# Kernel optimization log

Measured on AMD Instinct MI355X. Metric: run time of the kernel, lower is better.

The kernel has to match this reference:

```python
import jax, jax.numpy as jnp
import numpy as np

K_BINS = 2048
EMB_WIDTH = 512


def setup_inputs() -> dict:
    key = jax.random.key(0)
    k1, k2 = jax.random.split(key)
    x = jax.random.normal(k1, (16, EMB_WIDTH, 8192), dtype=jnp.float32)
    k = jax.random.normal(k2, (K_BINS, EMB_WIDTH), dtype=jnp.float32)
    return {"x": x, "k": k}


def reference(x, k):
    # BottleneckBlock.forward (eval path: codebook k given, no EMA update)
    N, W, T = x.shape  # W == emb_width
    # preprocess: [N, W, T] -> [N*T, W]
    xf = jnp.transpose(x, (0, 2, 1)).reshape(-1, W)
    n_el = float(xf.shape[0] * xf.shape[1])
    prenorm = jnp.linalg.norm(xf - jnp.mean(xf)) / np.float32(np.sqrt(n_el))
    # quantise: squared-distance via expansion, then argmin over codes
    x2 = jnp.sum(xf * xf, axis=-1, keepdims=True)          # [NT, 1]
    k2 = jnp.sum(k * k, axis=-1)                           # [K]
    dist = x2 - 2.0 * (xf @ k.T) + k2[None, :]             # [NT, K]
    x_l = jnp.argmin(dist, axis=-1)                        # [NT]
    fit = jnp.mean(jnp.min(dist, axis=-1))
    # dequantise: embedding gather
    x_d = k[x_l]                                           # [NT, W]
    # commit loss: ||sg(x_d) - x||^2 / numel (torch.norm(.)**2 == sum of squares)
    commit_loss = jnp.sum((jax.lax.stop_gradient(x_d) - xf) ** 2) / n_el
    # straight-through estimator
    x_q = xf + jax.lax.stop_gradient(x_d - xf)
    # postprocess: back to [N, T] and [N, W, T]
    x_l = x_l.reshape(N, T)
    x_q = jnp.transpose(x_q.reshape(N, T, W), (0, 2, 1))
    return (x_l, x_q, commit_loss, fit, prenorm)
```

## Files before the change

### kernel.cpp

```cpp
#include <hip/hip_runtime.h>

#define NBATCH 16
#define WEMB   512
#define TLEN   8192
#define KBINS  2048
#define NTROWS (NBATCH * TLEN)
#define XQN    (NBATCH * WEMB * TLEN)
#define XQ_OFF ((size_t)NTROWS)
#define SC_OFF ((size_t)NTROWS + (size_t)XQN)

#define FIX_CAP  65536
#define FIX2_CAP 8192
#define MARGIN1  0.2f
#define MARGIN2  0.02f

#define R      64
#define XS_ROW 512

typedef _Float16 half8 __attribute__((ext_vector_type(8)));
typedef __attribute__((ext_vector_type(8))) short short8;
typedef __attribute__((ext_vector_type(4))) float f32x4;

__device__ float          g_k2[KBINS];
__device__ double         g_fitp[2048];
__device__ double         g_pnp[2 * 2048];
__device__ int            g_idx[NTROWS];
__device__ int            g_list[FIX_CAP];
__device__ int            g_nfix;
__device__ int            g_list2[FIX2_CAP];
__device__ int            g_nfix2;
__device__ unsigned short g_kh[KBINS * WEMB];
__device__ unsigned short g_kbh[KBINS * WEMB];
__device__ unsigned short g_kbl[KBINS * WEMB];

static __device__ __forceinline__ unsigned short f2h(float f) {
  _Float16 h = (_Float16)f;
  unsigned short u;
  __builtin_memcpy(&u, &h, 2);
  return u;
}
static __device__ __forceinline__ unsigned short f2bf(float f) {
  unsigned int u;
  __builtin_memcpy(&u, &f, 4);
  return (unsigned short)((u + 0x7FFFu + ((u >> 16) & 1u)) >> 16);
}
static __device__ __forceinline__ float bf2f(unsigned short h) {
  unsigned int u = ((unsigned int)h) << 16;
  float f;
  __builtin_memcpy(&f, &u, 4);
  return f;
}

__global__ void zero_kernel() { g_nfix = 0; g_nfix2 = 0; }

__global__ __launch_bounds__(256) void k2_kernel(const float* __restrict__ k) {
  const int c = blockIdx.x * 4 + (threadIdx.x >> 6);
  const int lane = threadIdx.x & 63;
  const float4* kr = (const float4*)(k + (size_t)c * WEMB);
  float s = 0.f;
#pragma unroll
  for (int i = 0; i < 2; ++i) {
    float4 v = kr[lane + 64 * i];
    s += v.x * v.x + v.y * v.y + v.z * v.z + v.w * v.w;
  }
#pragma unroll
  for (int m = 1; m < 64; m <<= 1) s += __shfl_xor(s, m);
  if (lane == 0) g_k2[c] = s;
}

__global__ __launch_bounds__(256) void kprep_kernel(const float* __restrict__ k) {
  const int i = blockIdx.x * 256 + threadIdx.x;
  float4 v = ((const float4*)k)[i];
  ushort4 hf, hb, lb;
  hf.x = f2h(v.x); hb.x = f2bf(v.x); lb.x = f2bf(v.x - bf2f(hb.x));
  hf.y = f2h(v.y); hb.y = f2bf(v.y); lb.y = f2bf(v.y - bf2f(hb.y));
  hf.z = f2h(v.z); hb.z = f2bf(v.z); lb.z = f2bf(v.z - bf2f(hb.z));
  hf.w = f2h(v.w); hb.w = f2bf(v.w); lb.w = f2bf(v.w - bf2f(hb.w));
  ((ushort4*)g_kh)[i]  = hf;
  ((ushort4*)g_kbh)[i] = hb;
  ((ushort4*)g_kbl)[i] = lb;
}

__global__ __launch_bounds__(1024, 8) void vq_mfma(const float* __restrict__ x) {
  __shared__ unsigned short x_s[R * XS_ROW];
  __shared__ float  cand_d1[16][R];
  __shared__ float  cand_d2[16][R];
  __shared__ int    cand_i[16][R];
  __shared__ float  x2s[R];
  __shared__ double pnred[32];

  const int tid = threadIdx.x;
  const int wv = tid >> 6, lane = tid & 63;
  const int g = lane >> 4, i16 = lane & 15;
  const int rows0 = blockIdx.x * R;
  const int n = rows0 >> 13, t0 = rows0 & (TLEN - 1);
  const int swz = (i16 & 7) << 3;

  {
    float sv = 0.f, px = 0.f;
    const size_t xb = ((size_t)(n * WEMB + wv * 32)) * TLEN + (size_t)(t0 + lane);
    const int wsz = (lane & 7) << 3;
#pragma unroll
    for (int jg = 0; jg < 4; ++jg) {
      half8 h8;
#pragma unroll
      for (int j = 0; j < 8; ++j) {
        const float v = __builtin_nontemporal_load(&x[xb + (size_t)(jg * 8 + j) * TLEN]);
        h8[j] = (_Float16)v;
        px = fmaf(v, v, px);
        sv += v;
      }
      const int col = wv * 32 + jg * 8;
      *(half8*)&x_s[lane * XS_ROW + (col ^ wsz)] = h8;
    }
    cand_d1[wv][lane] = px;
    float svr = sv, pxr = px;
#pragma unroll
    for (int m = 1; m < 64; m <<= 1) { svr += __shfl_xor(svr, m); pxr += __shfl_xor(pxr, m); }
    if (lane == 0) { pnred[wv] = (double)svr; pnred[16 + wv] = (double)pxr; }
  }
  __syncthreads();
  if (tid < R) {
    float t = 0.f;
#pragma unroll
    for (int w16 = 0; w16 < 16; ++w16) t += cand_d1[w16][tid];
    x2s[tid] = t;
  }
  if (tid == 0) {
    double a = 0, b = 0;
#pragma unroll
    for (int w16 = 0; w16 < 16; ++w16) { a += pnred[w16]; b += pnred[16 + w16]; }
    g_pnp[2 * blockIdx.x] = a; g_pnp[2 * blockIdx.x + 1] = b;
  }
  __syncthreads();

  cand_d1[wv][lane] = 3.4e38f;
  cand_d2[wv][lane] = 3.4e38f;
  cand_i [wv][lane] = 0x7FFFFFFF;

  for (int cc = 0; cc < 8; ++cc) {
    const int cb = cc * 256 + wv * 16;
    f32x4 acc[4];
#pragma unroll
    for (int mt = 0; mt < 4; ++mt) acc[mt] = (f32x4){0.f, 0.f, 0.f, 0.f};

#pragma unroll 1
    for (int ks = 0; ks < 16; ++ks) {
      const half8 ak = *(const half8*)&g_kh[((size_t)(cb + i16)) * WEMB + (size_t)(ks * 32 + g * 8)];
#pragma unroll
      for (int mt = 0; mt < 4; ++mt) {
        const half8 bx = *(const half8*)&x_s[(mt * 16 + i16) * XS_ROW + ((ks * 32 + g * 8) ^ swz)];
        acc[mt] = __builtin_amdgcn_mfma_f32_16x16x32_f16(ak, bx, acc[mt], 0, 0, 0);
      }
    }

    float k2r[4];
#pragma unroll
    for (int r = 0; r < 4; ++r) k2r[r] = g_k2[cb + g * 4 + r];
#pragma unroll
    for (int mt = 0; mt < 4; ++mt) {
      const int row = mt * 16 + i16;
      const float xx = x2s[row];
      float e1 = 3.4e38f, e2 = 3.4e38f; int ei = 0x7FFFFFFF;
#pragma unroll
      for (int r = 0; r < 4; ++r) {
        const float d = fmaf(-2.f, acc[mt][r], xx) + k2r[r];
        const int code = cb + g * 4 + r;
        if (d < e1) { e2 = e1; e1 = d; ei = code; } else e2 = fminf(e2, d);
      }
#pragma unroll
      for (int m = 16; m <= 32; m <<= 1) {
        const float o1 = __shfl_xor(e1, m);
        const float o2 = __shfl_xor(e2, m);
        const int   oi = __shfl_xor(ei, m);
        if (o1 < e1)      { e2 = fminf(e1, o2); e1 = o1; ei = oi; }
        else if (o1 > e1) { e2 = fminf(e2, o1); }
        else              { e2 = fminf(e2, o2); if (oi < ei) ei = oi; }
      }
      if (g == 0) {
        const float c1 = cand_d1[wv][row], c2 = cand_d2[wv][row];
        const int ci = cand_i[wv][row];
        if (e1 < c1)      { cand_d2[wv][row] = fminf(c1, e2); cand_d1[wv][row] = e1; cand_i[wv][row] = ei; }
        else if (e1 > c1) { cand_d2[wv][row] = fminf(c2, e1); }
        else              { cand_d2[wv][row] = fminf(c2, e2); if (ei < ci) cand_i[wv][row] = ei; }
      }
    }
  }

  __syncthreads();
  if (tid < R) {
    float m1 = 3.4e38f, m2 = 3.4e38f; int mi = 0x7FFFFFFF;
#pragma unroll
    for (int w16 = 0; w16 < 16; ++w16) {
      const float c1 = cand_d1[w16][tid], c2 = cand_d2[w16][tid];
      const int ci = cand_i[w16][tid];
      if (c1 < m1)      { m2 = fminf(m1, c2); m1 = c1; mi = ci; }
      else if (c1 > m1) { m2 = fminf(m2, c1); }
      else              { m2 = fminf(m2, c2); if (ci < mi) mi = ci; }
    }
    const int grow = rows0 + tid;
    g_idx[grow] = mi;
    if (m2 - m1 < MARGIN1) {
      const int pos = atomicAdd(&g_nfix, 1);
      if (pos < FIX_CAP) g_list[pos] = grow;
    }
    double fs = (double)m1;
#pragma unroll
    for (int m = 1; m < 64; m <<= 1) fs += __shfl_xor(fs, m);
    if (tid == 0) g_fitp[blockIdx.x] = fs;
  }
}

__global__ __launch_bounds__(1024, 1) void fix1_mfma(const float* __restrict__ x) {
  __shared__ short  x_s[64 * 1024];
  __shared__ float  cand_d1[16][64];
  __shared__ float  cand_d2[16][64];
  __shared__ int    cand_i[16][64];
  __shared__ float  x2s[64];
  __shared__ float  rd1[64], rd2[64];
  __shared__ int    ri1[64];

  const int tid = threadIdx.x;
  const int wv = tid >> 6, lane = tid & 63;
  const int g = lane >> 4, i16 = lane & 15;
  const int swz = (i16 & 7) << 3;
  const int nfix = g_nfix < FIX_CAP ? g_nfix : FIX_CAP;

  for (int base = blockIdx.x * 64; base < nfix; base += gridDim.x * 64) {
    __syncthreads();
    if (tid < 64) { rd1[tid] = 3.4e38f; rd2[tid] = 3.4e38f; ri1[tid] = 0; }
    {
      const int rl = tid >> 4;
      int e = base + rl; if (e >= nfix) e = nfix - 1;
      const int row = g_list[e];
      const int n = row >> 13, t = row & (TLEN - 1);
      const int ks = tid & 15;
      const int wsz = (rl & 7) << 3;
      float px = 0.f;
#pragma unroll
      for (int jg = 0; jg < 4; ++jg) {
        short8 h8, l8;
#pragma unroll
        for (int j = 0; j < 8; ++j) {
          const int w = ks * 32 + jg * 8 + j;
          const float v = x[((size_t)(n * WEMB + w)) * TLEN + (size_t)t];
          const unsigned short h = f2bf(v);
          const unsigned short lo = f2bf(v - bf2f(h));
          h8[j] = (short)h; l8[j] = (short)lo;
          px = fmaf(v, v, px);
        }
        const int colh = ks * 64 + jg * 8;
        *(short8*)&x_s[rl * 1024 + (colh ^ wsz)] = h8;
        *(short8*)&x_s[rl * 1024 + ((colh + 32) ^ wsz)] = l8;
      }
#pragma unroll
      for (int m = 1; m < 16; m <<= 1) px += __shfl_xor(px, m);
      if (ks == 0) x2s[rl] = px;
    }
    __syncthreads();

    for (int cc = 0; cc < 4; ++cc) {
      const int cb = cc * 512 + wv * 32;
      f32x4 acc[4][2];
#pragma unroll
      for (int mt = 0; mt < 4; ++mt)
#pragma unroll
        for (int nt = 0; nt < 2; ++nt) acc[mt][nt] = (f32x4){0.f, 0.f, 0.f, 0.f};

#pragma unroll 1
      for (int ks = 0; ks < 16; ++ks) {
        short8 bh[2], bl[2];
#pragma unroll
        for (int nt = 0; nt < 2; ++nt) {
          const size_t bidx = ((size_t)(cb + nt * 16 + i16)) * WEMB + (size_t)(ks * 32 + g * 8);
          bh[nt] = *(const short8*)&g_kbh[bidx];
          bl[nt] = *(const short8*)&g_kbl[bidx];
        }
#pragma unroll
        for (int mt = 0; mt < 4; ++mt) {
          const int rbase = (mt * 16 + i16) * 1024 + (ks * 64);
          const short8 ah = *(const short8*)&x_s[rbase + ((g * 8) ^ swz)];
          const short8 al = *(const short8*)&x_s[rbase + ((32 + g * 8) ^ swz)];
          acc[mt][0] = __builtin_amdgcn_mfma_f32_16x16x32_bf16(ah, bh[0], acc[mt][0], 0, 0, 0);
          acc[mt][1] = __builtin_amdgcn_mfma_f32_16x16x32_bf16(ah, bh[1], acc[mt][1], 0, 0, 0);
          acc[mt][0] = __builtin_amdgcn_mfma_f32_16x16x32_bf16(ah, bl[0], acc[mt][0], 0, 0, 0);
          acc[mt][1] = __builtin_amdgcn_mfma_f32_16x16x32_bf16(ah, bl[1], acc[mt][1], 0, 0, 0);
          acc[mt][0] = __builtin_amdgcn_mfma_f32_16x16x32_bf16(al, bh[0], acc[mt][0], 0, 0, 0);
          acc[mt][1] = __builtin_amdgcn_mfma_f32_16x16x32_bf16(al, bh[1], acc[mt][1], 0, 0, 0);
        }
      }

      float k2v[2];
#pragma unroll
      for (int nt = 0; nt < 2; ++nt) k2v[nt] = g_k2[cb + nt * 16 + i16];
#pragma unroll
      for (int mt = 0; mt < 4; ++mt) {
#pragma unroll
        for (int rr = 0; rr < 4; ++rr) {
          const int row = mt * 16 + g * 4 + rr;
          const float xx = x2s[row];
          float e1 = 3.4e38f, e2 = 3.4e38f; int ei = 0x7FFFFFFF;
#pragma unroll
          for (int nt = 0; nt < 2; ++nt) {
            const float d = fmaf(-2.f, acc[mt][nt][rr], xx) + k2v[nt];
            const int code = cb + nt * 16 + i16;
            if (d < e1) { e2 = e1; e1 = d; ei = code; } else e2 = fminf(e2, d);
          }
#pragma unroll
          for (int m = 1; m < 16; m <<= 1) {
            const float o1 = __shfl_xor(e1, m);
            const float o2 = __shfl_xor(e2, m);
            const int   oi = __shfl_xor(ei, m);
            if (o1 < e1)      { e2 = fminf(e1, o2); e1 = o1; ei = oi; }
            else if (o1 > e1) { e2 = fminf(e2, o1); }
            else              { e2 = e1; if (oi < ei) ei = oi; }
          }
          if (i16 == 0) { cand_d1[wv][row] = e1; cand_d2[wv][row] = e2; cand_i[wv][row] = ei; }
        }
      }
      __syncthreads();
      if (tid < 64) {
        float m1 = rd1[tid], m2 = rd2[tid]; int mi = ri1[tid];
#pragma unroll
        for (int w16 = 0; w16 < 16; ++w16) {
          const float c1 = cand_d1[w16][tid], c2 = cand_d2[w16][tid];
          const int ci = cand_i[w16][tid];
          if (c1 < m1)      { m2 = fminf(m1, c2); m1 = c1; mi = ci; }
          else if (c1 > m1) { m2 = fminf(m2, c1); }
          else              { m2 = fminf(m2, c2); if (ci < mi) mi = ci; }
        }
        rd1[tid] = m1; rd2[tid] = m2; ri1[tid] = mi;
      }
      __syncthreads();
    }

    if (tid < 64) {
      const int e = base + tid;
      if (e < nfix) {
        const int row = g_list[e];
        g_idx[row] = ri1[tid];
        if (rd2[tid] - rd1[tid] < MARGIN2) {
          const int p = atomicAdd(&g_nfix2, 1);
          if (p < FIX2_CAP) g_list2[p] = row;
        }
      }
    }
  }
}

__global__ __launch_bounds__(256) void fix2_kernel(const float* __restrict__ x,
                                                   const float* __restrict__ k) {
  __shared__ float  xr[WEMB];
  __shared__ double rbd[4];
  __shared__ int    rbi[4];
  const int nf = g_nfix2 < FIX2_CAP ? g_nfix2 : FIX2_CAP;
  const int tid = threadIdx.x, lane = tid & 63, wv = tid >> 6;
  for (int e = blockIdx.x; e < nf; e += gridDim.x) {
    const int row = g_list2[e];
    const int n = row >> 13, t = row & (TLEN - 1);
    for (int w = tid; w < WEMB; w += 256)
      xr[w] = x[(size_t)(n * WEMB + w) * TLEN + (size_t)t];
    __syncthreads();
    double bd = 1e300; int bi = 0x7FFFFFFF;
    for (int p = 0; p < 8; ++p) {
      const int c = tid + 256 * p;
      const float* kc = k + (size_t)c * WEMB;
      double d = 0.0;
      for (int w = 0; w < WEMB; ++w) {
        const double df = (double)xr[w] - (double)kc[w];
        d = fma(df, df, d);
      }
      if (d < bd || (d == bd && c < bi)) { bd = d; bi = c; }
    }
#pragma unroll
    for (int m = 1; m < 64; m <<= 1) {
      const double od = __shfl_xor(bd, m);
      const int    oi = __shfl_xor(bi, m);
      if (od < bd || (od == bd && oi < bi)) { bd = od; bi = oi; }
    }
    if (lane == 0) { rbd[wv] = bd; rbi[wv] = bi; }
    __syncthreads();
    if (tid == 0) {
      double fb = rbd[0]; int fi = rbi[0];
#pragma unroll
      for (int v = 1; v < 4; ++v)
        if (rbd[v] < fb || (rbd[v] == fb && rbi[v] < fi)) { fb = rbd[v]; fi = rbi[v]; }
      g_idx[row] = fi;
    }
    __syncthreads();
  }
}

__global__ __launch_bounds__(256) void xl_kernel(float* __restrict__ out) {
  const int i = blockIdx.x * 256 + threadIdx.x;
  if (i < NTROWS) __builtin_nontemporal_store((float)g_idx[i], &out[i]);
}

__global__ __launch_bounds__(256) void xq_kernel(const float* __restrict__ k,
                                                 float* __restrict__ out) {
  __shared__ float tile[64][257];
  __shared__ int idxs[64];
  const int tb = blockIdx.x;
  const int n = tb >> 7, t0 = (tb & 127) << 6;
  const int tid = threadIdx.x, lane = tid & 63;
  if (tid < 64) idxs[tid] = g_idx[n * TLEN + t0 + tid];
  __syncthreads();
  for (int half = 0; half < 2; ++half) {
    const int w0 = half * 256;
    if (half) __syncthreads();
#pragma unroll 4
    for (int it = 0; it < 16; ++it) {
      const int r = (tid >> 6) + 4 * it;
      const float4 v = *(const float4*)&k[(size_t)idxs[r] * WEMB + (size_t)(w0 + lane * 4)];
      tile[r][lane * 4 + 0] = v.x; tile[r][lane * 4 + 1] = v.y;
      tile[r][lane * 4 + 2] = v.z; tile[r][lane * 4 + 3] = v.w;
    }
    __syncthreads();
#pragma unroll 4
    for (int it = 0; it < 64; ++it) {
      const int wl = it * 4 + (tid >> 6);
      __builtin_nontemporal_store(tile[lane][wl],
          &out[XQ_OFF + ((size_t)(n * WEMB + w0 + wl)) * TLEN + (size_t)(t0 + lane)]);
    }
  }
}

__global__ __launch_bounds__(256) void fin_kernel(float* __restrict__ out) {
  const int tid = threadIdx.x;
  double fs = 0, s = 0, s2 = 0;
  for (int i = tid; i < 2048; i += 256) {
    fs += g_fitp[i];
    s  += g_pnp[2 * i];
    s2 += g_pnp[2 * i + 1];
  }
#pragma unroll
  for (int m = 1; m < 64; m <<= 1) {
    fs += __shfl_xor(fs, m); s += __shfl_xor(s, m); s2 += __shfl_xor(s2, m);
  }
  __shared__ double red[12];
  const int wv = tid >> 6, lane = tid & 63;
  if (lane == 0) { red[wv] = fs; red[4 + wv] = s; red[8 + wv] = s2; }
  __syncthreads();
  if (tid == 0) {
    const double F  = red[0] + red[1] + red[2] + red[3];
    const double S  = red[4] + red[5] + red[6] + red[7];
    const double S2 = red[8] + red[9] + red[10] + red[11];
    const double nel = (double)NTROWS * (double)WEMB;
    const double mean = S / nel;
    double var = S2 / nel - mean * mean;
    if (var < 0) var = 0;
    out[SC_OFF + 0] = (float)(F / nel);
    out[SC_OFF + 1] = (float)(F / NTROWS);
    out[SC_OFF + 2] = (float)sqrt(var);
  }
}

extern "C" void kernel_launch(void* const* d_in, const int* in_sizes, int n_in,
                              void* d_out, int out_size, void* d_ws, size_t ws_size,
                              hipStream_t stream) {
  const float* x = (const float*)d_in[0];
  const float* k = (const float*)d_in[1];
  float* out = (float*)d_out;
  (void)d_ws; (void)ws_size; (void)in_sizes; (void)n_in; (void)out_size;

  hipLaunchKernelGGL(zero_kernel, dim3(1), dim3(1), 0, stream);
  hipLaunchKernelGGL(k2_kernel, dim3(KBINS / 4), dim3(256), 0, stream, k);
  hipLaunchKernelGGL(kprep_kernel, dim3(1024), dim3(256), 0, stream, k);
  hipLaunchKernelGGL(vq_mfma, dim3(NTROWS / R), dim3(1024), 0, stream, x);
  hipLaunchKernelGGL(fix1_mfma, dim3(512), dim3(1024), 0, stream, x);
  hipLaunchKernelGGL(fix2_kernel, dim3(1024), dim3(256), 0, stream, x, k);
  hipLaunchKernelGGL(xl_kernel, dim3(NTROWS / 256), dim3(256), 0, stream, out);
  hipLaunchKernelGGL(xq_kernel, dim3(2048), dim3(256), 0, stream, k, out);
  hipLaunchKernelGGL(fin_kernel, dim3(1), dim3(256), 0, stream, out);
}
```

Before: 945.5 us.

## Switch distance GEMM to 32x32x16 MFMA tiles with wider per-wave code blocks

The codebook-distance matmul moves from 16x16x32 f16 MFMA over 4 row tiles to 32x32x16 MFMA over 2 row tiles. Each wave now covers 32 codes per chunk in 4 chunks instead of 16 codes in 8. The change aims to cut the number of MFMA issues and LDS/global operand loads per FLOP, and to shrink the epilogue's cross-lane reduction to a single shuffle stage. In exchange the accumulators need more registers, which may lower occupancy, and the K loop runs twice as many iterations.

Result: slower. 1.127 ms (+19.2%).

```diff
diff --git a/kernel.cpp b/kernel.cpp
--- a/kernel.cpp
+++ b/kernel.cpp
@@ -18,8 +18,9 @@
 #define XS_ROW 512
 
 typedef _Float16 half8 __attribute__((ext_vector_type(8)));
-typedef __attribute__((ext_vector_type(8))) short short8;
-typedef __attribute__((ext_vector_type(4))) float f32x4;
+typedef __attribute__((ext_vector_type(8)))  short short8;
+typedef __attribute__((ext_vector_type(4)))  float f32x4;
+typedef __attribute__((ext_vector_type(16))) float f32x16;
 
 __device__ float          g_k2[KBINS];
 __device__ double         g_fitp[2048];
@@ -81,6 +82,36 @@
   ((ushort4*)g_kbl)[i] = lb;
 }
 
+#define EPIL32(ACC, TILE)                                                        \
+  { const int row = (TILE) * 32 + c32;                                           \
+    const float xx = x2s[row];                                                   \
+    float e1 = 3.4e38f, e2 = 3.4e38f; int ei = 0x7FFFFFFF;                       \
+    _Pragma("unroll")                                                            \
+    for (int q = 0; q < 4; ++q) {                                                \
+      const float4 kq = *(const float4*)&g_k2[cb + 8 * q + 4 * hi];              \
+      _Pragma("unroll")                                                          \
+      for (int e = 0; e < 4; ++e) {                                              \
+        const float kv = (e == 0) ? kq.x : (e == 1) ? kq.y : (e == 2) ? kq.z : kq.w; \
+        const float d = fmaf(-2.f, ACC[4 * q + e], xx) + kv;                     \
+        const int code = cb + 8 * q + 4 * hi + e;        \
+        if (d < e1) { e2 = e1; e1 = d; ei = code; } else e2 = fminf(e2, d);      \
+      }                                                                          \
+    }                                                                            \
+    { const float o1 = __shfl_xor(e1, 32);                                       \
+      const float o2 = __shfl_xor(e2, 32);                                       \
+      const int   oi = __shfl_xor(ei, 32);                                       \
+      if (o1 < e1)      { e2 = fminf(e1, o2); e1 = o1; ei = oi; }                \
+      else if (o1 > e1) { e2 = fminf(e2, o1); }                                  \
+      else              { e2 = fminf(e2, o2); if (oi < ei) ei = oi; }            \
+    }                                                                            \
+    if (hi == 0) {                \
+      const float c1 = cand_d1[wv][row], c2 = cand_d2[wv][row];                  \
+      const int ci = cand_i[wv][row];                                            \
+      if (e1 < c1)      { cand_d2[wv][row] = fminf(c1, e2); cand_d1[wv][row] = e1; cand_i[wv][row] = ei; } \
+      else if (e1 > c1) { cand_d2[wv][row] = fminf(c2, e1); }                    \
+      else              { cand_d2[wv][row] = fminf(c2, e2); if (ei < ci) cand_i[wv][row] = ei; } \
+    } }
+
 __global__ __launch_bounds__(1024, 8) void vq_mfma(const float* __restrict__ x) {
   __shared__ unsigned short x_s[R * XS_ROW];
   __shared__ float  cand_d1[16][R];
@@ -91,10 +122,10 @@
 
   const int tid = threadIdx.x;
   const int wv = tid >> 6, lane = tid & 63;
-  const int g = lane >> 4, i16 = lane & 15;
+  const int c32 = lane & 31, hi = lane >> 5;
   const int rows0 = blockIdx.x * R;
   const int n = rows0 >> 13, t0 = rows0 & (TLEN - 1);
-  const int swz = (i16 & 7) << 3;
+  const int swz32 = (c32 & 7) << 3;
 
   {
     float sv = 0.f, px = 0.f;
@@ -138,53 +169,24 @@
   cand_d2[wv][lane] = 3.4e38f;
   cand_i [wv][lane] = 0x7FFFFFFF;
 
-  for (int cc = 0; cc < 8; ++cc) {
-    const int cb = cc * 256 + wv * 16;
-    f32x4 acc[4];
-#pragma unroll
-    for (int mt = 0; mt < 4; ++mt) acc[mt] = (f32x4){0.f, 0.f, 0.f, 0.f};
+  for (int cc = 0; cc < 4; ++cc) {
+    const int cb = cc * 512 + wv * 32;
+    const unsigned short* kp = g_kh + ((size_t)(cb + c32)) * WEMB + (size_t)(hi * 8);
+    f32x16 acc0, acc1;
+#pragma unroll
+    for (int i = 0; i < 16; ++i) { acc0[i] = 0.f; acc1[i] = 0.f; }
 
 #pragma unroll 1
-    for (int ks = 0; ks < 16; ++ks) {
-      const half8 ak = *(const half8*)&g_kh[((size_t)(cb + i16)) * WEMB + (size_t)(ks * 32 + g * 8)];
-#pragma unroll
-      for (int mt = 0; mt < 4; ++mt) {
-        const half8 bx = *(const half8*)&x_s[(mt * 16 + i16) * XS_ROW + ((ks * 32 + g * 8) ^ swz)];
-        acc[mt] = __builtin_amdgcn_mfma_f32_16x16x32_f16(ak, bx, acc[mt], 0, 0, 0);
-      }
-    }
-
-    float k2r[4];
-#pragma unroll
-    for (int r = 0; r < 4; ++r) k2r[r] = g_k2[cb + g * 4 + r];
-#pragma unroll
-    for (int mt = 0; mt < 4; ++mt) {
-      const int row = mt * 16 + i16;
-      const float xx = x2s[row];
-      float e1 = 3.4e38f, e2 = 3.4e38f; int ei = 0x7FFFFFFF;
-#pragma unroll
-      for (int r = 0; r < 4; ++r) {
-        const float d = fmaf(-2.f, acc[mt][r], xx) + k2r[r];
-        const int code = cb + g * 4 + r;
-        if (d < e1) { e2 = e1; e1 = d; ei = code; } else e2 = fminf(e2, d);
-      }
-#pragma unroll
-      for (int m = 16; m <= 32; m <<= 1) {
-        const float o1 = __shfl_xor(e1, m);
-        const float o2 = __shfl_xor(e2, m);
-        const int   oi = __shfl_xor(ei, m);
-        if (o1 < e1)      { e2 = fminf(e1, o2); e1 = o1; ei = oi; }
-        else if (o1 > e1) { e2 = fminf(e2, o1); }
-        else              { e2 = fminf(e2, o2); if (oi < ei) ei = oi; }
-      }
-      if (g == 0) {
-        const float c1 = cand_d1[wv][row], c2 = cand_d2[wv][row];
-        const int ci = cand_i[wv][row];
-        if (e1 < c1)      { cand_d2[wv][row] = fminf(c1, e2); cand_d1[wv][row] = e1; cand_i[wv][row] = ei; }
-        else if (e1 > c1) { cand_d2[wv][row] = fminf(c2, e1); }
-        else              { cand_d2[wv][row] = fminf(c2, e2); if (ei < ci) cand_i[wv][row] = ei; }
-      }
-    }
+    for (int ks = 0; ks < 32; ++ks) {
+      const half8 ak  = *(const half8*)&kp[ks * 16];
+      const int   col = (ks * 16 + hi * 8) ^ swz32;
+      const half8 bx0 = *(const half8*)&x_s[c32 * XS_ROW + col];
+      const half8 bx1 = *(const half8*)&x_s[(32 + c32) * XS_ROW + col];
+      acc0 = __builtin_amdgcn_mfma_f32_32x32x16_f16(ak, bx0, acc0, 0, 0, 0);
+      acc1 = __builtin_amdgcn_mfma_f32_32x32x16_f16(ak, bx1, acc1, 0, 0, 0);
+    }
+    EPIL32(acc0, 0)
+    EPIL32(acc1, 1)
   }
 
   __syncthreads();
```

## Switch distance GEMM to 32x32x16 MFMA tiles with prefetched codebook fragments

Applied to the files above, without the earlier changes.

Each wave now computes a 32-row by 32-code tile with the 32x32x16 f16 MFMA instead of four 16x16x32 tiles over 16 codes, and waves are split 2x8 over rows and codes. Codebook fragments are software-prefetched one iteration ahead, and s_setprio is raised around the MFMAs. The argmin epilogue now needs only one cross-lane shuffle step, and k2 is read as float4. This is meant to cut LDS reads per MFMA and hide global-load latency, at the cost of more accumulator and prefetch registers.

New measurement: 1.464 ms. 54.8% more time.

```diff
diff --git a/kernel.cpp b/kernel.cpp
--- a/kernel.cpp
+++ b/kernel.cpp
@@ -18,8 +18,9 @@
 #define XS_ROW 512
 
 typedef _Float16 half8 __attribute__((ext_vector_type(8)));
-typedef __attribute__((ext_vector_type(8))) short short8;
-typedef __attribute__((ext_vector_type(4))) float f32x4;
+typedef __attribute__((ext_vector_type(8)))  short short8;
+typedef __attribute__((ext_vector_type(4)))  float f32x4;
+typedef __attribute__((ext_vector_type(16))) float f32x16;
 
 __device__ float          g_k2[KBINS];
 __device__ double         g_fitp[2048];
@@ -91,10 +92,12 @@
 
   const int tid = threadIdx.x;
   const int wv = tid >> 6, lane = tid & 63;
-  const int g = lane >> 4, i16 = lane & 15;
+  const int c32 = lane & 31, hi = lane >> 5;
+  const int wm = wv & 1, wn = wv >> 1;
   const int rows0 = blockIdx.x * R;
   const int n = rows0 >> 13, t0 = rows0 & (TLEN - 1);
-  const int swz = (i16 & 7) << 3;
+  const int swz32 = (c32 & 7) << 3;
+  const int bxbase = (wm * 32 + c32) * XS_ROW;
 
   {
     float sv = 0.f, px = 0.f;
@@ -139,51 +142,63 @@
   cand_i [wv][lane] = 0x7FFFFFFF;
 
   for (int cc = 0; cc < 8; ++cc) {
-    const int cb = cc * 256 + wv * 16;
-    f32x4 acc[4];
-#pragma unroll
-    for (int mt = 0; mt < 4; ++mt) acc[mt] = (f32x4){0.f, 0.f, 0.f, 0.f};
-
+    const int cb = cc * 256 + wn * 32;
+    const unsigned short* kp = g_kh + ((size_t)(cb + c32)) * WEMB + (size_t)(hi * 8);
+    f32x16 acc;
+#pragma unroll
+    for (int i = 0; i < 16; ++i) acc[i] = 0.f;
+
+    half8 a0 = *(const half8*)&kp[0];
+    half8 a1 = *(const half8*)&kp[16];
 #pragma unroll 1
-    for (int ks = 0; ks < 16; ++ks) {
-      const half8 ak = *(const half8*)&g_kh[((size_t)(cb + i16)) * WEMB + (size_t)(ks * 32 + g * 8)];
-#pragma unroll
-      for (int mt = 0; mt < 4; ++mt) {
-        const half8 bx = *(const half8*)&x_s[(mt * 16 + i16) * XS_ROW + ((ks * 32 + g * 8) ^ swz)];
-        acc[mt] = __builtin_amdgcn_mfma_f32_16x16x32_f16(ak, bx, acc[mt], 0, 0, 0);
-      }
-    }
-
-    float k2r[4];
-#pragma unroll
-    for (int r = 0; r < 4; ++r) k2r[r] = g_k2[cb + g * 4 + r];
-#pragma unroll
-    for (int mt = 0; mt < 4; ++mt) {
-      const int row = mt * 16 + i16;
-      const float xx = x2s[row];
-      float e1 = 3.4e38f, e2 = 3.4e38f; int ei = 0x7FFFFFFF;
-#pragma unroll
-      for (int r = 0; r < 4; ++r) {
-        const float d = fmaf(-2.f, acc[mt][r], xx) + k2r[r];
-        const int code = cb + g * 4 + r;
+    for (int kp2 = 0; kp2 < 16; ++kp2) {
+      const int ks0 = 2 * kp2, ks1 = 2 * kp2 + 1;
+      half8 n0, n1;
+      if (kp2 < 15) {
+        n0 = *(const half8*)&kp[(ks0 + 2) * 16];
+        n1 = *(const half8*)&kp[(ks1 + 2) * 16];
+      }
+      __builtin_amdgcn_s_setprio(1);
+      {
+        const half8 bx = *(const half8*)&x_s[bxbase + ((ks0 * 16 + hi * 8) ^ swz32)];
+        acc = __builtin_amdgcn_mfma_f32_32x32x16_f16(a0, bx, acc, 0, 0, 0);
+      }
+      {
+        const half8 bx = *(const half8*)&x_s[bxbase + ((ks1 * 16 + hi * 8) ^ swz32)];
+        acc = __builtin_amdgcn_mfma_f32_32x32x16_f16(a1, bx, acc, 0, 0, 0);
+      }
+      __builtin_amdgcn_s_setprio(0);
+      if (kp2 < 15) { a0 = n0; a1 = n1; }
+    }
+
+    const int row = wm * 32 + c32;
+    const float xx = x2s[row];
+    float e1 = 3.4e38f, e2 = 3.4e38f; int ei = 0x7FFFFFFF;
+#pragma unroll
+    for (int q = 0; q < 4; ++q) {
+      const float4 kq = *(const float4*)&g_k2[cb + 8 * q + 4 * hi];
+#pragma unroll
+      for (int e = 0; e < 4; ++e) {
+        const float kv = (e == 0) ? kq.x : (e == 1) ? kq.y : (e == 2) ? kq.z : kq.w;
+        const float d = fmaf(-2.f, acc[4 * q + e], xx) + kv;
+        const int code = cb + 8 * q + 4 * hi + e;
         if (d < e1) { e2 = e1; e1 = d; ei = code; } else e2 = fminf(e2, d);
       }
-#pragma unroll
-      for (int m = 16; m <= 32; m <<= 1) {
-        const float o1 = __shfl_xor(e1, m);
-        const float o2 = __shfl_xor(e2, m);
-        const int   oi = __shfl_xor(ei, m);
-        if (o1 < e1)      { e2 = fminf(e1, o2); e1 = o1; ei = oi; }
-        else if (o1 > e1) { e2 = fminf(e2, o1); }
-        else              { e2 = fminf(e2, o2); if (oi < ei) ei = oi; }
-      }
-      if (g == 0) {
-        const float c1 = cand_d1[wv][row], c2 = cand_d2[wv][row];
-        const int ci = cand_i[wv][row];
-        if (e1 < c1)      { cand_d2[wv][row] = fminf(c1, e2); cand_d1[wv][row] = e1; cand_i[wv][row] = ei; }
-        else if (e1 > c1) { cand_d2[wv][row] = fminf(c2, e1); }
-        else              { cand_d2[wv][row] = fminf(c2, e2); if (ei < ci) cand_i[wv][row] = ei; }
-      }
+    }
+    {
+      const float o1 = __shfl_xor(e1, 32);
+      const float o2 = __shfl_xor(e2, 32);
+      const int   oi = __shfl_xor(ei, 32);
+      if (o1 < e1)      { e2 = fminf(e1, o2); e1 = o1; ei = oi; }
+      else if (o1 > e1) { e2 = fminf(e2, o1); }
+      else              { e2 = fminf(e2, o2); if (oi < ei) ei = oi; }
+    }
+    if (hi == 0) {
+      const float c1 = cand_d1[wv][row], c2 = cand_d2[wv][row];
+      const int ci = cand_i[wv][row];
+      if (e1 < c1)      { cand_d2[wv][row] = fminf(c1, e2); cand_d1[wv][row] = e1; cand_i[wv][row] = ei; }
+      else if (e1 > c1) { cand_d2[wv][row] = fminf(c2, e1); }
+      else              { cand_d2[wv][row] = fminf(c2, e2); if (ei < ci) cand_i[wv][row] = ei; }
     }
   }
 
```
